# Performance work log

Measured on AMD Instinct MI355X. Metric: run time of the kernel, lower is better.

## Reference

```python
import jax, jax.numpy as jnp
import numpy as np
import math

DIM = 1024
K = 3
NUM_LAYERS = 1
RES_SCALE = 1.0 / math.sqrt(NUM_LAYERS)


def rmsnorm(x, gamma):
    # F.normalize(x, dim=-1) * sqrt(dim) * (gamma + 1)
    n = jnp.sqrt(jnp.sum(x * x, axis=-1, keepdims=True))
    return x / jnp.maximum(n, 1e-12) * (x.shape[-1] ** 0.5) * (gamma + 1.0)


def causal_dwconv(x, w_dw, b_dw, w_pw, b_pw):
    # x: [B, L, D]; w_dw: [D, 1, K]; w_pw: [D, D]
    xt = jnp.transpose(x, (0, 2, 1))                     # [B, D, L]
    xt = jnp.pad(xt, ((0, 0), (0, 0), (K - 1, 0)))       # causal left pad
    y = jax.lax.conv_general_dilated(
        xt, w_dw, window_strides=(1,), padding='VALID',
        feature_group_count=xt.shape[1],
        dimension_numbers=('NCH', 'OIH', 'NCH'))          # [B, D, L]
    y = y + b_dw[None, :, None]
    y = jnp.transpose(y, (0, 2, 1))                       # [B, L, D]
    return jnp.einsum('bld,ed->ble', y, w_pw) + b_pw      # 1x1 conv


def log_g(x):
    return jnp.where(x >= 0, jnp.log(jax.nn.relu(x) + 0.5), -jax.nn.softplus(-x))


def heinsen_scan_log(log_coeffs, log_values):
    # h_t = exp(a*_t + logcumsumexp(log_values - a*))
    a_star = jnp.cumsum(log_coeffs, axis=1)
    log_h = a_star + jax.lax.cumlogsumexp(log_values - a_star, axis=1)
    return jnp.exp(log_h)


def min_gru(x, w_hg):
    # x: [B, L, D]; w_hg: [2D, D] (no bias, expansion_factor=1 -> to_out is identity)
    hg = jnp.einsum('bld,ed->ble', x, w_hg)
    hidden, gate = jnp.split(hg, 2, axis=-1)
    log_coeffs = -jax.nn.softplus(gate)        # log(1 - z)
    log_values = -jax.nn.softplus(-gate) + log_g(hidden)  # log z + log g(h~)
    out = heinsen_scan_log(log_coeffs, log_values)         # [B, L, D]
    next_hidden = out[:, -1:]
    return out, next_hidden


def setup_inputs() -> dict:
    key = jax.random.key(0)
    ks = jax.random.split(key, 12)
    D = DIM
    s = 0.02
    return {
        'x': jax.random.normal(ks[0], (4, 4096, D), jnp.float32),
        'conv_dw_w': jax.random.normal(ks[1], (D, 1, K), jnp.float32) * s,
        'conv_dw_b': jax.random.normal(ks[2], (D,), jnp.float32) * s,
        'conv_pw_w': jax.random.normal(ks[3], (D, D), jnp.float32) * s,
        'conv_pw_b': jax.random.normal(ks[4], (D,), jnp.float32) * s,
        'conv_norm_g': jax.random.normal(ks[5], (D,), jnp.float32) * s,
        'gru_norm_g': jax.random.normal(ks[6], (D,), jnp.float32) * s,
        'gru_w': jax.random.normal(ks[7], (2 * D, D), jnp.float32) * s,
        'ff_norm_g': jax.random.normal(ks[8], (D,), jnp.float32) * s,
        'ff_w1': jax.random.normal(ks[9], (4 * D, D), jnp.float32) * s,
        'ff_b1': jax.random.normal(ks[10], (4 * D,), jnp.float32) * s,
        'ff_w2': jax.random.normal(ks[11], (D, 4 * D), jnp.float32) * s,
        'ff_b2': jnp.zeros((D,), jnp.float32),
    }


def reference(x, conv_dw_w, conv_dw_b, conv_pw_w, conv_pw_b, conv_norm_g,
              gru_norm_g, gru_w, ff_norm_g, ff_w1, ff_b1, ff_w2, ff_b2):
    # Conv branch (residual)
    x = causal_dwconv(rmsnorm(x, conv_norm_g), conv_dw_w, conv_dw_b,
                      conv_pw_w, conv_pw_b) * RES_SCALE + x
    # MinGRU branch (residual); dropout is identity at inference
    gru_out, next_hidden = min_gru(rmsnorm(x, gru_norm_g), gru_w)
    x = gru_out * RES_SCALE + x
    # FeedForward branch (residual), exact GELU
    h = rmsnorm(x, ff_norm_g)
    h = jax.nn.gelu(jnp.einsum('bld,ed->ble', h, ff_w1) + ff_b1, approximate=False)
    h = jnp.einsum('ble,de->bld', h, ff_w2) + ff_b2
    x = h * RES_SCALE + x
    return x, next_hidden
```

## Files before the change

kernel.cpp:

```cpp
#include <hip/hip_runtime.h>

typedef __attribute__((ext_vector_type(8))) short short8;
typedef __attribute__((ext_vector_type(4))) float floatx4;

#define D_   1024
#define L_   4096
#define B_   4
#define T_   16384
#define NCH  32
#define CHL  128

__device__ __forceinline__ ushort f2bf(float f) {
  unsigned u = __float_as_uint(f);
  u += 0x7fffu + ((u >> 16) & 1u);
  return (ushort)(u >> 16);
}
__device__ __forceinline__ float bf2f(ushort u) {
  return __uint_as_float(((unsigned)u) << 16);
}

__device__ __forceinline__ void gl2lds(const ushort* g, ushort* l) {
  __builtin_amdgcn_global_load_lds(
      (const __attribute__((address_space(1))) unsigned int*)g,
      (__attribute__((address_space(3))) unsigned int*)l, 16, 0, 0);
}

__global__ __launch_bounds__(256) void cvt_bf(const float* __restrict__ s,
                                              ushort* __restrict__ d, int n4) {
  int i = blockIdx.x * 256 + threadIdx.x;
  if (i >= n4) return;
  float4 v = ((const float4*)s)[i];
  ushort4 o;
  o.x = f2bf(v.x); o.y = f2bf(v.y); o.z = f2bf(v.z); o.w = f2bf(v.w);
  ((ushort4*)d)[i] = o;
}

__global__ __launch_bounds__(256) void rms_scale(const float* __restrict__ x,
                                                 const float* __restrict__ g,
                                                 ushort* __restrict__ z) {
  int t = blockIdx.x;
  float4 v = ((const float4*)(x + (size_t)t * D_))[threadIdx.x];
  float s = v.x * v.x + v.y * v.y + v.z * v.z + v.w * v.w;
#pragma unroll
  for (int off = 32; off > 0; off >>= 1) s += __shfl_xor(s, off, 64);
  __shared__ float red[4];
  if ((threadIdx.x & 63) == 0) red[threadIdx.x >> 6] = s;
  __syncthreads();
  float iv = 32.0f / fmaxf(sqrtf(red[0] + red[1] + red[2] + red[3]), 1e-12f);
  float4 gg = ((const float4*)g)[threadIdx.x];
  ushort4 o;
  o.x = f2bf(v.x * iv * (gg.x + 1.f));
  o.y = f2bf(v.y * iv * (gg.y + 1.f));
  o.z = f2bf(v.z * iv * (gg.z + 1.f));
  o.w = f2bf(v.w * iv * (gg.w + 1.f));
  ((ushort4*)(z + (size_t)t * D_))[threadIdx.x] = o;
}

__global__ __launch_bounds__(256) void dwconv_k(const float* __restrict__ x,
                                                const float* __restrict__ wdw,
                                                const float* __restrict__ bdw,
                                                const float* __restrict__ gm,
                                                ushort* __restrict__ y) {
  int t = blockIdx.x;
  int c4 = threadIdx.x << 2;
  int l = t & (L_ - 1);
  const float* p0 = x + (size_t)t * D_ + c4;
  float4 v0 = *(const float4*)p0;
  float4 v1 = {0.f, 0.f, 0.f, 0.f}, v2 = {0.f, 0.f, 0.f, 0.f};
  if (l >= 1) v1 = *(const float4*)(p0 - D_);
  if (l >= 2) v2 = *(const float4*)(p0 - 2 * D_);
  float s0 = v0.x * v0.x + v0.y * v0.y + v0.z * v0.z + v0.w * v0.w;
  float s1 = v1.x * v1.x + v1.y * v1.y + v1.z * v1.z + v1.w * v1.w;
  float s2 = v2.x * v2.x + v2.y * v2.y + v2.z * v2.z + v2.w * v2.w;
#pragma unroll
  for (int off = 32; off > 0; off >>= 1) {
    s0 += __shfl_xor(s0, off, 64);
    s1 += __shfl_xor(s1, off, 64);
    s2 += __shfl_xor(s2, off, 64);
  }
  __shared__ float r0[4], r1[4], r2[4];
  if ((threadIdx.x & 63) == 0) {
    int w = threadIdx.x >> 6;
    r0[w] = s0; r1[w] = s1; r2[w] = s2;
  }
  __syncthreads();
  float i0 = 32.0f / fmaxf(sqrtf(r0[0] + r0[1] + r0[2] + r0[3]), 1e-12f);
  float i1 = 32.0f / fmaxf(sqrtf(r1[0] + r1[1] + r1[2] + r1[3]), 1e-12f);
  float i2 = 32.0f / fmaxf(sqrtf(r2[0] + r2[1] + r2[2] + r2[3]), 1e-12f);
  float a0[4] = {v0.x, v0.y, v0.z, v0.w};
  float a1[4] = {v1.x, v1.y, v1.z, v1.w};
  float a2[4] = {v2.x, v2.y, v2.z, v2.w};
  ushort r[4];
#pragma unroll
  for (int j = 0; j < 4; ++j) {
    int d = c4 + j;
    float w0 = wdw[d * 3 + 0], w1 = wdw[d * 3 + 1], w2 = wdw[d * 3 + 2];
    float s = w2 * a0[j] * i0 + w1 * a1[j] * i1 + w0 * a2[j] * i2;
    s = s * (gm[d] + 1.0f) + bdw[d];
    r[j] = f2bf(s);
  }
  ushort4 o; o.x = r[0]; o.y = r[1]; o.z = r[2]; o.w = r[3];
  *(ushort4*)(y + (size_t)t * D_ + c4) = o;
}


#define READ_A(BUFO, MQ)                                                      \
  _Pragma("unroll") for (int mf_ = 0; mf_ < 4; ++mf_) {                       \
    av[2 * mf_]     = *(const short8*)(pA + (BUFO) + (MQ) + mf_ * 1024 + o0); \
    av[2 * mf_ + 1] = *(const short8*)(pA + (BUFO) + (MQ) + mf_ * 1024 + o1); \
  }

#define READ_B(BUFO, NH)                                                      \
  _Pragma("unroll") for (int nf_ = 0; nf_ < 2; ++nf_) {                       \
    bv[(NH) * 4 + 2 * nf_] =                                                  \
        *(const short8*)(pB + (BUFO) + (NH) * 2048 + nf_ * 1024 + o0);        \
    bv[(NH) * 4 + 2 * nf_ + 1] =                                              \
        *(const short8*)(pB + (BUFO) + (NH) * 2048 + nf_ * 1024 + o1);        \
  }

#define MFMA_Q(MB, NB)                                                        \
  __builtin_amdgcn_s_setprio(1);                                              \
  _Pragma("unroll") for (int mf_ = 0; mf_ < 4; ++mf_) {                       \
    _Pragma("unroll") for (int nf_ = 0; nf_ < 2; ++nf_) {                     \
      floatx4 c_ = acc[(MB) + mf_][(NB) + nf_];                               \
      c_ = __builtin_amdgcn_mfma_f32_16x16x32_bf16(                           \
          av[2 * mf_], bv[((NB) + nf_) * 2], c_, 0, 0, 0);                    \
      c_ = __builtin_amdgcn_mfma_f32_16x16x32_bf16(                           \
          av[2 * mf_ + 1], bv[((NB) + nf_) * 2 + 1], c_, 0, 0, 0);            \
      acc[(MB) + mf_][(NB) + nf_] = c_;                                       \
    }                                                                         \
  }                                                                           \
  __builtin_amdgcn_s_setprio(0)

#define BAR_LGKM()                                    \
  __builtin_amdgcn_s_barrier();                       \
  asm volatile("s_waitcnt lgkmcnt(0)" ::: "memory");  \
  __builtin_amdgcn_sched_barrier(0)

#define BAR_END()               \
  __builtin_amdgcn_s_barrier(); \
  __builtin_amdgcn_sched_barrier(0)

template <int MODE>
__global__ __launch_bounds__(512, 2) void gemm256(
    const ushort* __restrict__ A, const ushort* __restrict__ W,
    const float* __restrict__ bias, const float* __restrict__ resid,
    float* __restrict__ outF, ushort* __restrict__ outB, int M, int N, int K) {
  __shared__ ushort lds[65536];
  const int tid = threadIdx.x;

  const int nx = gridDim.x;
  const int lxs = 31 - __clz(nx);
  const int lin = blockIdx.x + blockIdx.y * nx;
  const int cpx = nx << 3;
  const int wg = (lin & 7) * cpx + (lin >> 3);
  const int bm = (wg >> lxs) << 8;
  const int bn = (wg & (nx - 1)) << 8;

  const int lane = tid & 63, wave = tid >> 6;
  const int wm = (wave >> 2) & 1;
  const int wn = wave & 3;
  const int fr = lane & 15, fq = lane >> 4;

  const int srow = tid >> 3;
  const int kcs = (tid & 7) ^ (srow & 7);
  const ushort* gA = A + (size_t)(bm + srow) * K + kcs * 8;
  const ushort* gB = W + (size_t)(bn + srow) * K + kcs * 8;
  ushort* ldst = lds + tid * 8;

  const ushort* pA = lds + (size_t)(wm * 128 + fr) * 64;
  const ushort* pB = lds + 16384 + (size_t)(wn * 64 + fr) * 64;
  const int o0 = (fq ^ (fr & 7)) * 8;
  const int o1 = o0 ^ 32;

  floatx4 acc[8][4];
#pragma unroll
  for (int i = 0; i < 8; ++i)
#pragma unroll
    for (int j = 0; j < 4; ++j) acc[i][j] = {0.f, 0.f, 0.f, 0.f};
  short8 av[8], bv[8];

  auto stageA = [&](int buf, int half, int kt) {
    const ushort* s = gA + (size_t)(half * 128) * K + kt * 64;
    ushort* d = ldst + buf * 32768 + half * 8192;
    gl2lds(s, d);
    gl2lds(s + (size_t)64 * K, d + 4096);
  };
  auto stageB = [&](int buf, int half, int kt) {
    const ushort* s = gB + (size_t)(half * 128) * K + kt * 64;
    ushort* d = ldst + buf * 32768 + 16384 + half * 8192;
    gl2lds(s, d);
    gl2lds(s + (size_t)64 * K, d + 4096);
  };

  const int nt = K >> 6;

  stageA(0, 0, 0); stageA(0, 1, 0);
  stageB(0, 0, 0); stageB(0, 1, 0);
  stageB(1, 0, 1); stageB(1, 1, 1);
  asm volatile("s_waitcnt vmcnt(4)" ::: "memory");
  __builtin_amdgcn_s_barrier();
  __builtin_amdgcn_sched_barrier(0);

  for (int m = 0; m < nt; m += 2) {
    const bool more = (m + 2 < nt);
    READ_A(0, 0);
    READ_B(0, 0);
    stageA(1, 0, m + 1);
    BAR_LGKM();
    MFMA_Q(0, 0);
    BAR_END();

    READ_B(0, 1);
    stageA(1, 1, m + 1);
    BAR_LGKM();
    MFMA_Q(0, 2);
    BAR_END();

    READ_A(0, 4096);
    if (more) stageB(0, 0, m + 2);
    BAR_LGKM();
    MFMA_Q(4, 2);
    BAR_END();

    if (more) {
      stageB(0, 1, m + 2);
      asm volatile("s_waitcnt vmcnt(4)" ::: "memory");
    } else {
      asm volatile("s_waitcnt vmcnt(0)" ::: "memory");
    }
    __builtin_amdgcn_s_barrier();
    __builtin_amdgcn_sched_barrier(0);
    MFMA_Q(4, 0);
    BAR_END();

    READ_A(32768, 0);
    READ_B(32768, 0);
    if (more) stageA(0, 0, m + 2);
    BAR_LGKM();
    MFMA_Q(0, 0);
    BAR_END();

    READ_B(32768, 1);
    if (more) stageA(0, 1, m + 2);
    BAR_LGKM();
    MFMA_Q(0, 2);
    BAR_END();

    READ_A(32768, 4096);
    if (more) stageB(1, 0, m + 3);
    BAR_LGKM();
    MFMA_Q(4, 2);
    BAR_END();

    if (more) {
      stageB(1, 1, m + 3);
      asm volatile("s_waitcnt vmcnt(4)" ::: "memory");
    } else {
      asm volatile("s_waitcnt vmcnt(0)" ::: "memory");
    }
    __builtin_amdgcn_s_barrier();
    __builtin_amdgcn_sched_barrier(0);
    MFMA_Q(4, 0);
    BAR_END();
  }

  const int rowb = bm + wm * 128 + fq * 4;
  const int colb = bn + wn * 64 + fr;
#pragma unroll
  for (int nf = 0; nf < 4; ++nf) {
    const int colg = colb + nf * 16;
    const float bvs = (MODE == 4) ? 0.f : bias[colg];
#pragma unroll
    for (int mf = 0; mf < 8; ++mf) {
#pragma unroll
      for (int r = 0; r < 4; ++r) {
        const int rowg = rowb + mf * 16 + r;
        const size_t idx = (size_t)rowg * N + colg;
        float v = acc[mf][nf][r];
        if (MODE == 0) {
          outF[idx] = v + bvs + resid[idx];
        } else if (MODE == 2) {
          v += bvs;
          float u = 1.5957691216f * (v + 0.044715f * v * v * v);
          v = v / (1.f + __expf(-u));
          outB[idx] = f2bf(v);
        } else {
          float o;
          if (colg < 1024)
            o = (v >= 0.f) ? (v + 0.5f) : (1.f / (1.f + __expf(-v)));
          else
            o = 1.f / (1.f + __expf(v));
          outB[idx] = f2bf(o);
        }
      }
    }
  }
}

__global__ __launch_bounds__(256) void scan_p1(const ushort* __restrict__ hg,
                                               float* __restrict__ Ag,
                                               float* __restrict__ Bg) {
  int blk = blockIdx.x;
  int dt = blk & 3, ch = (blk >> 2) & 31, b = blk >> 7;
  int d = (dt << 8) + threadIdx.x;
  const ushort* p = hg + (size_t)(b * L_ + ch * CHL) * 2048 + d;
  float A = 1.f, Bv = 0.f;
  for (int s = 0; s < CHL; ++s) {
    float g = bf2f(p[0]), a = bf2f(p[1024]);
    p += 2048;
    A *= a;
    Bv = fmaf(a, Bv, (1.f - a) * g);
  }
  size_t o = (size_t)((b * NCH + ch) * D_) + d;
  Ag[o] = A; Bg[o] = Bv;
}

__global__ __launch_bounds__(256) void scan_p2(const float* __restrict__ Ag,
                                               const float* __restrict__ Bg,
                                               float* __restrict__ Pre) {
  int dt = blockIdx.x & 3, b = blockIdx.x >> 2;
  int d = (dt << 8) + threadIdx.x;
  float h = 0.f;
  for (int c = 0; c < NCH; ++c) {
    size_t i = (size_t)((b * NCH + c) * D_) + d;
    Pre[i] = h;
    h = fmaf(Ag[i], h, Bg[i]);
  }
}

__global__ __launch_bounds__(256) void scan_p3(const ushort* __restrict__ hg,
                                               const float* __restrict__ Pre,
                                               float* __restrict__ xio,
                                               float* __restrict__ nh) {
  int blk = blockIdx.x;
  int dt = blk & 3, ch = (blk >> 2) & 31, b = blk >> 7;
  int d = (dt << 8) + threadIdx.x;
  const ushort* p = hg + (size_t)(b * L_ + ch * CHL) * 2048 + d;
  float* q = xio + (size_t)(b * L_ + ch * CHL) * D_ + d;
  float h = Pre[(size_t)((b * NCH + ch) * D_) + d];
  for (int s = 0; s < CHL; ++s) {
    float g = bf2f(p[0]), a = bf2f(p[1024]);
    p += 2048;
    h = fmaf(a, h, (1.f - a) * g);
    *q = h + *q;
    q += D_;
  }
  if (ch == NCH - 1) nh[(b << 10) + d] = h;
}

extern "C" void kernel_launch(void* const* d_in, const int* in_sizes, int n_in,
                              void* d_out, int out_size, void* d_ws, size_t ws_size,
                              hipStream_t stream) {
  const float* x   = (const float*)d_in[0];
  const float* cdw = (const float*)d_in[1];
  const float* cdb = (const float*)d_in[2];
  const float* cpw = (const float*)d_in[3];
  const float* cpb = (const float*)d_in[4];
  const float* cng = (const float*)d_in[5];
  const float* gng = (const float*)d_in[6];
  const float* gw  = (const float*)d_in[7];
  const float* fng = (const float*)d_in[8];
  const float* fw1 = (const float*)d_in[9];
  const float* fb1 = (const float*)d_in[10];
  const float* fw2 = (const float*)d_in[11];
  const float* fb2 = (const float*)d_in[12];
  float* out = (float*)d_out;
  char* ws = (char*)d_ws;

  ushort* wpw_b = (ushort*)(ws + 0);
  ushort* wgr_b = (ushort*)(ws + 2097152);
  ushort* wf1_b = (ushort*)(ws + 6291456);
  ushort* wf2_b = (ushort*)(ws + 14680064);
  float*  Ag    = (float*) (ws + 23134208);
  float*  Bg    = (float*) (ws + 23658496);
  float*  Pre   = (float*) (ws + 24182784);
  ushort* zbuf  = (ushort*)(ws + 24707072);
  ushort* hg    = (ushort*)(ws + 58261504);
  ushort* h1    = (ushort*)(ws + 58261504);
  float*  nh    = out + (size_t)T_ * D_;

  cvt_bf<<<dim3(1024), 256, 0, stream>>>(cpw, wpw_b, 262144);
  cvt_bf<<<dim3(2048), 256, 0, stream>>>(gw,  wgr_b, 524288);
  cvt_bf<<<dim3(4096), 256, 0, stream>>>(fw1, wf1_b, 1048576);
  cvt_bf<<<dim3(4096), 256, 0, stream>>>(fw2, wf2_b, 1048576);

  dwconv_k<<<dim3(T_), 256, 0, stream>>>(x, cdw, cdb, cng, zbuf);
  gemm256<0><<<dim3(4, 64), 512, 0, stream>>>(zbuf, wpw_b, cpb, x, out, nullptr, T_, 1024, 1024);

  rms_scale<<<dim3(T_), 256, 0, stream>>>(out, gng, zbuf);
  gemm256<4><<<dim3(8, 64), 512, 0, stream>>>(zbuf, wgr_b, nullptr, nullptr, nullptr, hg, T_, 2048, 1024);
  scan_p1<<<dim3(512), 256, 0, stream>>>(hg, Ag, Bg);
  scan_p2<<<dim3(16), 256, 0, stream>>>(Ag, Bg, Pre);
  scan_p3<<<dim3(512), 256, 0, stream>>>(hg, Pre, out, nh);

  rms_scale<<<dim3(T_), 256, 0, stream>>>(out, fng, zbuf);
  gemm256<2><<<dim3(16, 64), 512, 0, stream>>>(zbuf, wf1_b, fb1, nullptr, nullptr, h1, T_, 4096, 1024);
  gemm256<0><<<dim3(4, 64), 512, 0, stream>>>(h1, wf2_b, fb2, out, out, nullptr, T_, 1024, 4096);
}
```

Measured before the change: 715.3 us.

## Merge GEMM main-loop phases and drop explicit LDS waitcnt before MFMAs

Each half-iteration of the GEMM main loop goes from four barrier-separated phases to three. The two MFMA quadrants that shared A fragments now run back to back in one phase. The explicit `s_waitcnt lgkmcnt(0)` after the mid-phase barrier is replaced by a plain asm barrier, so the compiler inserts LDS waits where the data dependence needs them. Global-to-LDS staging calls are regrouped so the vmcnt counting still waits on the same loads. The aim is less barrier and wait overhead per K-step, at the cost of higher register pressure or reduced latency hiding if the compiler places waits too early.

Result: no change. 718.7 us (+0.5%).

```diff
diff --git a/kernel.cpp b/kernel.cpp
--- a/kernel.cpp
+++ b/kernel.cpp
@@ -132,13 +132,9 @@
   }                                                                           \
   __builtin_amdgcn_s_setprio(0)
 
-#define BAR_LGKM()                                    \
-  __builtin_amdgcn_s_barrier();                       \
-  asm volatile("s_waitcnt lgkmcnt(0)" ::: "memory");  \
-  __builtin_amdgcn_sched_barrier(0)
-
-#define BAR_END()               \
-  __builtin_amdgcn_s_barrier(); \
+#define PHASE_MID() asm volatile("s_barrier" ::: "memory")
+#define PHASE_END()                        \
+  asm volatile("s_barrier" ::: "memory");  \
   __builtin_amdgcn_sched_barrier(0)
 
 template <int MODE>
@@ -199,70 +195,59 @@
   stageB(0, 0, 0); stageB(0, 1, 0);
   stageB(1, 0, 1); stageB(1, 1, 1);
   asm volatile("s_waitcnt vmcnt(4)" ::: "memory");
-  __builtin_amdgcn_s_barrier();
-  __builtin_amdgcn_sched_barrier(0);
+  PHASE_END();
 
   for (int m = 0; m < nt; m += 2) {
     const bool more = (m + 2 < nt);
     READ_A(0, 0);
     READ_B(0, 0);
-    stageA(1, 0, m + 1);
-    BAR_LGKM();
+    stageA(1, 0, m + 1); stageA(1, 1, m + 1);
+    PHASE_MID();
     MFMA_Q(0, 0);
-    BAR_END();
+    PHASE_END();
 
     READ_B(0, 1);
-    stageA(1, 1, m + 1);
-    BAR_LGKM();
+    if (more) stageB(0, 0, m + 2);
+    PHASE_MID();
     MFMA_Q(0, 2);
-    BAR_END();
+    PHASE_END();
 
     READ_A(0, 4096);
-    if (more) stageB(0, 0, m + 2);
-    BAR_LGKM();
-    MFMA_Q(4, 2);
-    BAR_END();
-
     if (more) {
       stageB(0, 1, m + 2);
       asm volatile("s_waitcnt vmcnt(4)" ::: "memory");
     } else {
       asm volatile("s_waitcnt vmcnt(0)" ::: "memory");
     }
-    __builtin_amdgcn_s_barrier();
-    __builtin_amdgcn_sched_barrier(0);
+    PHASE_MID();
+    MFMA_Q(4, 2);
     MFMA_Q(4, 0);
-    BAR_END();
+    PHASE_END();
 
     READ_A(32768, 0);
     READ_B(32768, 0);
-    if (more) stageA(0, 0, m + 2);
-    BAR_LGKM();
+    if (more) { stageA(0, 0, m + 2); stageA(0, 1, m + 2); }
+    PHASE_MID();
     MFMA_Q(0, 0);
-    BAR_END();
+    PHASE_END();
 
     READ_B(32768, 1);
-    if (more) stageA(0, 1, m + 2);
-    BAR_LGKM();
+    if (more) stageB(1, 0, m + 3);
+    PHASE_MID();
     MFMA_Q(0, 2);
-    BAR_END();
+    PHASE_END();
 
     READ_A(32768, 4096);
-    if (more) stageB(1, 0, m + 3);
-    BAR_LGKM();
-    MFMA_Q(4, 2);
-    BAR_END();
-
     if (more) {
       stageB(1, 1, m + 3);
       asm volatile("s_waitcnt vmcnt(4)" ::: "memory");
     } else {
       asm volatile("s_waitcnt vmcnt(0)" ::: "memory");
     }
-    __builtin_amdgcn_s_barrier();
-    __builtin_amdgcn_sched_barrier(0);
+    PHASE_MID();
+    MFMA_Q(4, 2);
     MFMA_Q(4, 0);
-    BAR_END();
+    PHASE_END();
   }
 
   const int rowb = bm + wm * 128 + fq * 4;
```

## Restructure GEMM main loop with separate register fragments for prefetched LDS reads

Applied to the files above, without the earlier changes.

Splits the A and B fragment registers into separate even and odd buffers so that LDS reads for the next quadrant (and the next k-tile's first A fragment) can be issued ahead of the MFMAs that use the current ones. The intent is to overlap ds_read latency with MFMA work. It also merges the two B global stages into one slot and swaps the s_barrier builtin for inline asm. This raises VGPR pressure (four A and four B fragment arrays), which could cause spills or lower occupancy under launch_bounds(512,2). The barrier and wait ordering changes also risk LDS race issues.

Result: slower. 1.799 ms (+151.5%).

```diff
diff --git a/kernel.cpp b/kernel.cpp
--- a/kernel.cpp
+++ b/kernel.cpp
@@ -104,41 +104,39 @@
 }
 
 
-#define READ_A(BUFO, MQ)                                                      \
-  _Pragma("unroll") for (int mf_ = 0; mf_ < 4; ++mf_) {                       \
-    av[2 * mf_]     = *(const short8*)(pA + (BUFO) + (MQ) + mf_ * 1024 + o0); \
-    av[2 * mf_ + 1] = *(const short8*)(pA + (BUFO) + (MQ) + mf_ * 1024 + o1); \
-  }
-
-#define READ_B(BUFO, NH)                                                      \
-  _Pragma("unroll") for (int nf_ = 0; nf_ < 2; ++nf_) {                       \
-    bv[(NH) * 4 + 2 * nf_] =                                                  \
-        *(const short8*)(pB + (BUFO) + (NH) * 2048 + nf_ * 1024 + o0);        \
-    bv[(NH) * 4 + 2 * nf_ + 1] =                                              \
-        *(const short8*)(pB + (BUFO) + (NH) * 2048 + nf_ * 1024 + o1);        \
-  }
-
-#define MFMA_Q(MB, NB)                                                        \
-  __builtin_amdgcn_s_setprio(1);                                              \
-  _Pragma("unroll") for (int mf_ = 0; mf_ < 4; ++mf_) {                       \
-    _Pragma("unroll") for (int nf_ = 0; nf_ < 2; ++nf_) {                     \
-      floatx4 c_ = acc[(MB) + mf_][(NB) + nf_];                               \
-      c_ = __builtin_amdgcn_mfma_f32_16x16x32_bf16(                           \
-          av[2 * mf_], bv[((NB) + nf_) * 2], c_, 0, 0, 0);                    \
-      c_ = __builtin_amdgcn_mfma_f32_16x16x32_bf16(                           \
-          av[2 * mf_ + 1], bv[((NB) + nf_) * 2 + 1], c_, 0, 0, 0);            \
-      acc[(MB) + mf_][(NB) + nf_] = c_;                                       \
-    }                                                                         \
-  }                                                                           \
+#define DS_A(DST, PB, MQ)                                                    \
+  _Pragma("unroll") for (int mf_ = 0; mf_ < 4; ++mf_) {                      \
+    DST[2 * mf_]     = *(const short8*)((PB) + (MQ) + mf_ * 1024 + o0);      \
+    DST[2 * mf_ + 1] = *(const short8*)((PB) + (MQ) + mf_ * 1024 + o1);      \
+  }
+
+#define DS_B(DST, PB, NH)                                                    \
+  _Pragma("unroll") for (int nf_ = 0; nf_ < 2; ++nf_) {                      \
+    DST[2 * nf_]     = *(const short8*)((PB) + (NH) * 2048 + nf_ * 1024 + o0); \
+    DST[2 * nf_ + 1] = *(const short8*)((PB) + (NH) * 2048 + nf_ * 1024 + o1); \
+  }
+
+#define MFMA_C(AS, BS, MB, NB)                                               \
+  __builtin_amdgcn_s_setprio(1);                                             \
+  _Pragma("unroll") for (int mf_ = 0; mf_ < 4; ++mf_) {                      \
+    _Pragma("unroll") for (int nf_ = 0; nf_ < 2; ++nf_) {                    \
+      floatx4 c_ = acc[(MB) + mf_][(NB) + nf_];                              \
+      c_ = __builtin_amdgcn_mfma_f32_16x16x32_bf16(AS[2 * mf_],              \
+             BS[2 * nf_], c_, 0, 0, 0);                                      \
+      c_ = __builtin_amdgcn_mfma_f32_16x16x32_bf16(AS[2 * mf_ + 1],          \
+             BS[2 * nf_ + 1], c_, 0, 0, 0);                                  \
+      acc[(MB) + mf_][(NB) + nf_] = c_;                                      \
+    }                                                                        \
+  }                                                                          \
   __builtin_amdgcn_s_setprio(0)
 
 #define BAR_LGKM()                                    \
-  __builtin_amdgcn_s_barrier();                       \
+  asm volatile("s_barrier" ::: "memory");             \
   asm volatile("s_waitcnt lgkmcnt(0)" ::: "memory");  \
   __builtin_amdgcn_sched_barrier(0)
 
-#define BAR_END()               \
-  __builtin_amdgcn_s_barrier(); \
+#define BAR_END()                          \
+  asm volatile("s_barrier" ::: "memory");  \
   __builtin_amdgcn_sched_barrier(0)
 
 template <int MODE>
@@ -168,8 +166,10 @@
   const ushort* gB = W + (size_t)(bn + srow) * K + kcs * 8;
   ushort* ldst = lds + tid * 8;
 
-  const ushort* pA = lds + (size_t)(wm * 128 + fr) * 64;
-  const ushort* pB = lds + 16384 + (size_t)(wn * 64 + fr) * 64;
+  const ushort* pA0 = lds + (size_t)(wm * 128 + fr) * 64;
+  const ushort* pB0 = lds + 16384 + (size_t)(wn * 64 + fr) * 64;
+  const ushort* pA1 = pA0 + 32768;
+  const ushort* pB1 = pB0 + 32768;
   const int o0 = (fq ^ (fr & 7)) * 8;
   const int o1 = o0 ^ 32;
 
@@ -178,7 +178,8 @@
   for (int i = 0; i < 8; ++i)
 #pragma unroll
     for (int j = 0; j < 4; ++j) acc[i][j] = {0.f, 0.f, 0.f, 0.f};
-  short8 av[8], bv[8];
+  short8 aE0[8], aE1[8], aO0[8], aO1[8];
+  short8 bE0[4], bE1[4], bO0[4], bO1[4];
 
   auto stageA = [&](int buf, int half, int kt) {
     const ushort* s = gA + (size_t)(half * 128) * K + kt * 64;
@@ -199,69 +200,57 @@
   stageB(0, 0, 0); stageB(0, 1, 0);
   stageB(1, 0, 1); stageB(1, 1, 1);
   asm volatile("s_waitcnt vmcnt(4)" ::: "memory");
-  __builtin_amdgcn_s_barrier();
-  __builtin_amdgcn_sched_barrier(0);
+  BAR_END();
+  DS_A(aE0, pA0, 0);
 
   for (int m = 0; m < nt; m += 2) {
     const bool more = (m + 2 < nt);
-    READ_A(0, 0);
-    READ_B(0, 0);
+    DS_B(bE0, pB0, 0); DS_B(bE1, pB0, 1);
     stageA(1, 0, m + 1);
     BAR_LGKM();
-    MFMA_Q(0, 0);
-    BAR_END();
-
-    READ_B(0, 1);
+    MFMA_C(aE0, bE0, 0, 0);
+    BAR_END();
+    DS_A(aE1, pA0, 4096);
     stageA(1, 1, m + 1);
     BAR_LGKM();
-    MFMA_Q(0, 2);
-    BAR_END();
-
-    READ_A(0, 4096);
-    if (more) stageB(0, 0, m + 2);
-    BAR_LGKM();
-    MFMA_Q(4, 2);
-    BAR_END();
-
+    MFMA_C(aE0, bE1, 0, 2);
+    BAR_END();
     if (more) {
-      stageB(0, 1, m + 2);
+      stageB(0, 0, m + 2); stageB(0, 1, m + 2);
       asm volatile("s_waitcnt vmcnt(4)" ::: "memory");
     } else {
       asm volatile("s_waitcnt vmcnt(0)" ::: "memory");
     }
-    __builtin_amdgcn_s_barrier();
-    __builtin_amdgcn_sched_barrier(0);
-    MFMA_Q(4, 0);
-    BAR_END();
-
-    READ_A(32768, 0);
-    READ_B(32768, 0);
+    BAR_LGKM();
+    MFMA_C(aE1, bE1, 4, 2);
+    BAR_END();
+    DS_A(aO0, pA1, 0);
+    BAR_LGKM();
+    MFMA_C(aE1, bE0, 4, 0);
+    BAR_END();
+
+    DS_B(bO0, pB1, 0); DS_B(bO1, pB1, 1);
     if (more) stageA(0, 0, m + 2);
     BAR_LGKM();
-    MFMA_Q(0, 0);
-    BAR_END();
-
-    READ_B(32768, 1);
+    MFMA_C(aO0, bO0, 0, 0);
+    BAR_END();
+    DS_A(aO1, pA1, 4096);
     if (more) stageA(0, 1, m + 2);
     BAR_LGKM();
-    MFMA_Q(0, 2);
-    BAR_END();
-
-    READ_A(32768, 4096);
-    if (more) stageB(1, 0, m + 3);
-    BAR_LGKM();
-    MFMA_Q(4, 2);
-    BAR_END();
-
+    MFMA_C(aO0, bO1, 0, 2);
+    BAR_END();
     if (more) {
-      stageB(1, 1, m + 3);
+      stageB(1, 0, m + 3); stageB(1, 1, m + 3);
       asm volatile("s_waitcnt vmcnt(4)" ::: "memory");
     } else {
       asm volatile("s_waitcnt vmcnt(0)" ::: "memory");
     }
-    __builtin_amdgcn_s_barrier();
-    __builtin_amdgcn_sched_barrier(0);
-    MFMA_Q(4, 0);
+    BAR_LGKM();
+    MFMA_C(aO1, bO1, 4, 2);
+    BAR_END();
+    if (more) { DS_A(aE0, pA0, 0); }
+    BAR_LGKM();
+    MFMA_C(aO1, bO0, 4, 0);
     BAR_END();
   }
 
```
